# Kernel optimization log

Hardware: AMD Instinct MI355X
Metric: run time of the kernel (lower is better)

Reference implementation:

```python
import jax, jax.numpy as jnp
import numpy as np

WIDTH = 256
FREQS = 10
INPUT_WIDTH = 3 + 3 * 2 * FREQS  # 63


def embed_point(point, freqs):
    # point: [N, 3] -> [N, 3*(1+2*freqs)]
    linear = point[..., None]                                  # [N, 3, 1]
    scales = jnp.exp2(jnp.arange(freqs, dtype=point.dtype))    # [freqs]
    angles = linear * scales                                   # [N, 3, freqs]
    emb = jnp.concatenate((linear, jnp.sin(angles), jnp.cos(angles)), axis=-1)
    return emb.reshape(*point.shape[:-1], 3 * (1 + 2 * freqs))


def _xavier(key, fan_in, fan_out):
    limit = jnp.sqrt(6.0 / (fan_in + fan_out)).astype(jnp.float32)
    return jax.random.uniform(key, (fan_in, fan_out), jnp.float32, -limit, limit)


def setup_inputs() -> dict:
    key = jax.random.key(0)
    keys = jax.random.split(key, 20)
    N = 524288
    point = jax.random.normal(keys[0], (N, 3), dtype=jnp.float32)
    dims = [
        (INPUT_WIDTH, WIDTH), (WIDTH, WIDTH), (WIDTH, WIDTH), (WIDTH, WIDTH),
        (WIDTH, WIDTH), (WIDTH + INPUT_WIDTH, WIDTH), (WIDTH, WIDTH),
        (WIDTH, WIDTH), (WIDTH, 4),
    ]
    inp = {"point": point}
    for i, (fi, fo) in enumerate(dims):
        inp[f"w{i}"] = _xavier(keys[1 + i], fi, fo)
        inp[f"b{i}"] = jnp.zeros((fo,), dtype=jnp.float32)
    return inp


def reference(point, w0, b0, w1, b1, w2, b2, w3, b3, w4, b4,
              w5, b5, w6, b6, w7, b7, w8, b8):
    inp = embed_point(point, FREQS)                 # [N, 63]
    x = jax.nn.relu(inp @ w0 + b0)
    x = jax.nn.relu(x @ w1 + b1)
    x = jax.nn.relu(x @ w2 + b2)
    x = jax.nn.relu(x @ w3 + b3)
    x = jax.nn.relu(x @ w4 + b4)
    x = jax.nn.relu(jnp.concatenate((x, inp), -1) @ w5 + b5)  # skip concat
    x = jax.nn.relu(x @ w6 + b6)
    x = jax.nn.relu(x @ w7 + b7)
    return x @ w8 + b8                              # [N, 4]
```

## Files before the change

kernel.cpp:

```cpp
#include <hip/hip_runtime.h>
#include <math.h>


typedef __attribute__((ext_vector_type(8))) short short8;
typedef __attribute__((ext_vector_type(4))) float f32x4;
typedef __attribute__((ext_vector_type(16))) float f32x16;

struct WPtrs { const float* w[8]; };
struct BPtrs { const float* b[8]; };

#define INV2PI 0.15915494309189533577f

#define PK_L0 0
#define PK_L1 16384
#define PK_L2 81920
#define PK_L3 147456
#define PK_L4 212992
#define PK_L5 278528
#define PK_L6 360448
#define PK_L7 425984
#define PK_W8 491520
#define PK_TOTAL 495616

__device__ __forceinline__ unsigned short f2bf(float v) {
  unsigned u = __float_as_uint(v);
  u = u + 0x7fffu + ((u >> 16) & 1u);
  return (unsigned short)(u >> 16);
}
__device__ __forceinline__ float bf_lo(unsigned u) { return __uint_as_float(u << 16); }
__device__ __forceinline__ float bf_hi(unsigned u) { return __uint_as_float(u & 0xffff0000u); }

__device__ __forceinline__ unsigned cvtpk(float a, float b) {
#if __has_builtin(__builtin_amdgcn_cvt_pk_bf16_f32)
  typedef __attribute__((ext_vector_type(2))) __bf16 bf16x2_t;
  bf16x2_t r = __builtin_amdgcn_cvt_pk_bf16_f32(a, b);
  return __builtin_bit_cast(unsigned, r);
#else
  unsigned ua = __float_as_uint(a);
  ua += 0x7fffu + ((ua >> 16) & 1u);
  unsigned ub = __float_as_uint(b);
  ub += 0x7fffu + ((ub >> 16) & 1u);
#if __has_builtin(__builtin_amdgcn_perm)
  return __builtin_amdgcn_perm(ub, ua, 0x07060302u);
#else
  return (ua >> 16) | (ub & 0xffff0000u);
#endif
#endif
}

__device__ __forceinline__ float fractf_(float x) {
#if __has_builtin(__builtin_amdgcn_fract_f32)
  return __builtin_amdgcn_fract_f32(x);
#else
  return x - floorf(x);
#endif
}
__device__ __forceinline__ float sin_rev(float rev) {
#if __has_builtin(__builtin_amdgcn_sinf)
  return __builtin_amdgcn_sinf(rev);
#else
  return __sinf(rev * 6.283185307179586f);
#endif
}

__device__ __forceinline__ float embval(int f, float c0, float c1, float c2,
                                        float x0, float x1, float x2) {
  if (f >= 63) return 0.0f;
  int d = (f >= 21 ? 1 : 0) + (f >= 42 ? 1 : 0);
  int r = f - d * 21;
  float c = (d == 0) ? c0 : (d == 1 ? c1 : c2);
  float x = (d == 0) ? x0 : (d == 1 ? x1 : x2);
  bool isc = r > 10;
  int e = isc ? (r - 11) : (r - 1);
  float rev = fractf_(ldexpf(x, e) + (isc ? 0.25f : 0.0f));
  float s = sin_rev(rev);
  return (r == 0) ? c : s;
}

__device__ __forceinline__ f32x16 mfma32(short8 a, short8 b, f32x16 c) {
  return __builtin_amdgcn_mfma_f32_32x32x16_bf16(a, b, c, 0, 0, 0);
}
__device__ __forceinline__ f32x4 mfma16(short8 a, short8 b, f32x4 c) {
  return __builtin_amdgcn_mfma_f32_16x16x32_bf16(a, b, c, 0, 0, 0);
}

__global__ void pack_weights(WPtrs W, const float* __restrict__ w8,
                             unsigned short* __restrict__ out) {
  int idx = blockIdx.x * 256 + threadIdx.x;
  if (idx >= PK_TOTAL) return;
  float v;
  if (idx >= PK_W8) {
    int t = idx - PK_W8;
    int j = t >> 8, k = t & 255;
    v = (j < 4) ? w8[k * 4 + j] : 0.0f;
  } else {
    int e = idx & 15;
    int blk = idx >> 4;
    int ch = blk & 255;
    int kkg = blk >> 8;
    int l, kk0;
    if      (kkg < 4)   { l = 0; kk0 = 0;   }
    else if (kkg < 20)  { l = 1; kk0 = 4;   }
    else if (kkg < 36)  { l = 2; kk0 = 20;  }
    else if (kkg < 52)  { l = 3; kk0 = 36;  }
    else if (kkg < 68)  { l = 4; kk0 = 52;  }
    else if (kkg < 88)  { l = 5; kk0 = 68;  }
    else if (kkg < 104) { l = 6; kk0 = 88;  }
    else                { l = 7; kk0 = 104; }
    int k = (kkg - kk0) * 16 + e;
    const int realK[8] = {63, 256, 256, 256, 256, 319, 256, 256};
    v = (k < realK[l]) ? W.w[l][k * 256 + ch] : 0.0f;
  }
  out[idx] = f2bf(v);
}

template <int KKA, int PAB, int KKB, bool RB>
__device__ __forceinline__ void do_layer32(
    const unsigned short* srcA, const unsigned short* srcB,
    const unsigned short* __restrict__ wblk,
    const float* __restrict__ bias,
    unsigned short* dst, int wr, int wc, int n, int h, unsigned swz) {
  f32x16 acc[4][2];
#pragma unroll
  for (int mt = 0; mt < 4; ++mt)
#pragma unroll
    for (int q = 0; q < 4; ++q) {
      f32x4 bq = *reinterpret_cast<const f32x4*>(bias + wr * 128 + mt * 32 + q * 8 + h * 4);
#pragma unroll
      for (int nt = 0; nt < 2; ++nt)
#pragma unroll
        for (int r = 0; r < 4; ++r)
          acc[mt][nt][q * 4 + r] = bq[r];
    }

  const char* wb = (const char*)wblk;
  const unsigned aoff = (unsigned)((wr * 128 + n) * 32 + h * 16);
  const char* rA = (const char*)srcA + (unsigned)((wc * 64 + n) * PAB);

#define LOAD_A(KK, A0, A1, A2, A3) do {                              \
    const char* ap_ = wb + (aoff + (unsigned)((KK) * 8192));         \
    A0 = *reinterpret_cast<const short8*>(ap_);                      \
    A1 = *reinterpret_cast<const short8*>(ap_ + 1024);               \
    A2 = *reinterpret_cast<const short8*>(ap_ + 2048);               \
    A3 = *reinterpret_cast<const short8*>(ap_ + 3072);               \
  } while (0)
#define LOAD_B(KK, B0, B1) do {                                      \
    unsigned off_ = ((unsigned)((KK) * 32 + h * 16)) ^ swz;          \
    const char* p_ = rA + off_;                                      \
    B0 = *reinterpret_cast<const short8*>(p_);                       \
    B1 = *reinterpret_cast<const short8*>(p_ + 32 * PAB);            \
  } while (0)
#define MFMA8(A0, A1, A2, A3, B0, B1) do {                           \
    acc[0][0] = mfma32(A0, B0, acc[0][0]);                           \
    acc[0][1] = mfma32(A0, B1, acc[0][1]);                           \
    acc[1][0] = mfma32(A1, B0, acc[1][0]);                           \
    acc[1][1] = mfma32(A1, B1, acc[1][1]);                           \
    acc[2][0] = mfma32(A2, B0, acc[2][0]);                           \
    acc[2][1] = mfma32(A2, B1, acc[2][1]);                           \
    acc[3][0] = mfma32(A3, B0, acc[3][0]);                           \
    acc[3][1] = mfma32(A3, B1, acc[3][1]);                           \
  } while (0)

  short8 a0e, a1e, a2e, a3e, b0e, b1e;
  short8 a0o, a1o, a2o, a3o, b0o, b1o;
  LOAD_B(0, b0e, b1e);
  LOAD_A(0, a0e, a1e, a2e, a3e);

#pragma unroll
  for (int kk = 0; kk < KKA; ++kk) {
    if ((kk & 1) == 0) {
      if (kk + 1 < KKA) {
        LOAD_B(kk + 1, b0o, b1o);
        LOAD_A(kk + 1, a0o, a1o, a2o, a3o);
      }
      __builtin_amdgcn_sched_barrier(0);
      __builtin_amdgcn_s_setprio(1);
      MFMA8(a0e, a1e, a2e, a3e, b0e, b1e);
      __builtin_amdgcn_s_setprio(0);
      __builtin_amdgcn_sched_barrier(0);
    } else {
      if (kk + 1 < KKA) {
        LOAD_B(kk + 1, b0e, b1e);
        LOAD_A(kk + 1, a0e, a1e, a2e, a3e);
      }
      __builtin_amdgcn_sched_barrier(0);
      __builtin_amdgcn_s_setprio(1);
      MFMA8(a0o, a1o, a2o, a3o, b0o, b1o);
      __builtin_amdgcn_s_setprio(0);
      __builtin_amdgcn_sched_barrier(0);
    }
  }

  if (KKB > 0) {
    const char* rB = (const char*)srcB + (unsigned)((wc * 64 + n) * 128);
#pragma unroll
    for (int kl = 0; kl < KKB; ++kl) {
      const char* ap = wb + (aoff + (unsigned)((KKA + kl) * 8192));
      short8 a0 = *reinterpret_cast<const short8*>(ap);
      short8 a1 = *reinterpret_cast<const short8*>(ap + 1024);
      short8 a2 = *reinterpret_cast<const short8*>(ap + 2048);
      short8 a3 = *reinterpret_cast<const short8*>(ap + 3072);
      unsigned off = ((unsigned)(kl * 32 + h * 16)) ^ swz;
      const char* p = rB + off;
      short8 b0 = *reinterpret_cast<const short8*>(p);
      short8 b1 = *reinterpret_cast<const short8*>(p + 32 * 128);
      __builtin_amdgcn_s_setprio(1);
      MFMA8(a0, a1, a2, a3, b0, b1);
      __builtin_amdgcn_s_setprio(0);
    }
  }
#undef LOAD_A
#undef LOAD_B
#undef MFMA8

  if (RB) __syncthreads();
  char* d0 = (char*)dst + (unsigned)((wc * 64 + n) * 512);
#pragma unroll
  for (int mt = 0; mt < 4; ++mt)
#pragma unroll
    for (int q = 0; q < 4; ++q) {
      unsigned soff = ((unsigned)(wr * 256 + mt * 64 + q * 16 + h * 8)) ^ swz;
      char* sp = d0 + soff;
#pragma unroll
      for (int nt = 0; nt < 2; ++nt) {
        float x0 = fmaxf(acc[mt][nt][q * 4 + 0], 0.0f);
        float x1 = fmaxf(acc[mt][nt][q * 4 + 1], 0.0f);
        float x2 = fmaxf(acc[mt][nt][q * 4 + 2], 0.0f);
        float x3 = fmaxf(acc[mt][nt][q * 4 + 3], 0.0f);
        uint2 pr;
        pr.x = cvtpk(x0, x1);
        pr.y = cvtpk(x2, x3);
        *reinterpret_cast<uint2*>(sp + nt * 16384) = pr;
      }
    }
  __syncthreads();
}

__launch_bounds__(256, 2)
__global__ void mlp_mfma(const float* __restrict__ pts, long N,
                         BPtrs B, const float* __restrict__ b8,
                         const unsigned short* __restrict__ wpk,
                         float* __restrict__ out) {
  extern __shared__ unsigned short smem[];
  unsigned short* act = smem;
  unsigned short* emb = smem + 32768;
  const int tid = threadIdx.x;
  const int w = tid >> 6, lane = tid & 63;
  const int n = lane & 31, h = lane >> 5;
  const int wr = w >> 1, wc = w & 1;
  const unsigned swz = (unsigned)((n & 7) << 4);
  const long pbase = (long)blockIdx.x * 128;

  {
    const int pt = tid >> 1, fg = tid & 1;
    const long pg = pbase + pt;
    float c0 = 0.f, c1 = 0.f, c2 = 0.f;
    if (pg < N) {
      const float* pp = pts + pg * 3;
      c0 = __builtin_nontemporal_load(pp);
      c1 = __builtin_nontemporal_load(pp + 1);
      c2 = __builtin_nontemporal_load(pp + 2);
    }
    float x0 = c0 * INV2PI, x1 = c1 * INV2PI, x2 = c2 * INV2PI;
    const unsigned sw = (unsigned)((pt & 7) << 4);
    char* rowp = (char*)emb + (unsigned)(pt * 128);
#pragma unroll
    for (int jb = 0; jb < 2; ++jb) {
      unsigned pk[8];
#pragma unroll
      for (int i = 0; i < 16; i += 2) {
        int f0 = fg * 32 + jb * 16 + i;
        float v0 = embval(f0,     c0, c1, c2, x0, x1, x2);
        float v1 = embval(f0 + 1, c0, c1, c2, x0, x1, x2);
        pk[i >> 1] = cvtpk(v0, v1);
      }
      unsigned base = (unsigned)(fg * 64 + jb * 32);
      *reinterpret_cast<uint4*>(rowp + (base ^ sw)) =
          uint4{pk[0], pk[1], pk[2], pk[3]};
      *reinterpret_cast<uint4*>(rowp + ((base + 16) ^ sw)) =
          uint4{pk[4], pk[5], pk[6], pk[7]};
    }
  }
  __syncthreads();

  do_layer32<4,  128, 0, false>(emb, nullptr, wpk + PK_L0, B.b[0], act, wr, wc, n, h, swz);
  do_layer32<16, 512, 0, true >(act, nullptr, wpk + PK_L1, B.b[1], act, wr, wc, n, h, swz);
  do_layer32<16, 512, 0, true >(act, nullptr, wpk + PK_L2, B.b[2], act, wr, wc, n, h, swz);
  do_layer32<16, 512, 0, true >(act, nullptr, wpk + PK_L3, B.b[3], act, wr, wc, n, h, swz);
  do_layer32<16, 512, 0, true >(act, nullptr, wpk + PK_L4, B.b[4], act, wr, wc, n, h, swz);
  do_layer32<16, 512, 4, true >(act, emb,     wpk + PK_L5, B.b[5], act, wr, wc, n, h, swz);
  do_layer32<16, 512, 0, true >(act, nullptr, wpk + PK_L6, B.b[6], act, wr, wc, n, h, swz);
  do_layer32<16, 512, 0, true >(act, nullptr, wpk + PK_L7, B.b[7], act, wr, wc, n, h, swz);

  {
    const int l16 = lane & 15, quad = lane >> 4;
    const unsigned short* w8b = wpk + PK_W8 + (unsigned)(l16 * 256 + quad * 8);
    short8 wf[8];
#pragma unroll
    for (int kk = 0; kk < 8; ++kk)
      wf[kk] = *reinterpret_cast<const short8*>(w8b + kk * 32);
    f32x4 bb = *reinterpret_cast<const f32x4*>(b8);
#pragma unroll
    for (int it = 0; it < 2; ++it) {
      const int pt = w * 32 + it * 16 + l16;
      const char* ba = (const char*)act + (unsigned)(pt * 512);
      f32x4 a4 = {0.f, 0.f, 0.f, 0.f};
#pragma unroll
      for (int kk = 0; kk < 8; ++kk) {
        unsigned off = ((unsigned)(kk * 64 + quad * 16)) ^ swz;
        short8 b = *reinterpret_cast<const short8*>(ba + off);
        a4 = mfma16(wf[kk], b, a4);
      }
      if (quad == 0) {
        long pg = pbase + pt;
        f32x4 v = a4 + bb;
        if (pg < N)
          __builtin_nontemporal_store(v, reinterpret_cast<f32x4*>(out + pg * 4));
      }
    }
  }
}

__device__ __forceinline__ unsigned pk2s(float a, float b) {
  return (unsigned)f2bf(a) | ((unsigned)f2bf(b) << 16);
}
__device__ __forceinline__ void fb_seg(const unsigned short* src, int kRows,
                                       const float* __restrict__ wr,
                                       int lane, int ps, float acc[4][16]) {
#pragma unroll 4
  for (int k = 0; k < kRows; ++k) {
    const float* p = wr + k * 256 + lane;
    float w0 = p[0], w1 = p[64], w2 = p[128], w3 = p[192];
    const uint4* xr = reinterpret_cast<const uint4*>(src + ((k << 6) + ps));
    uint4 q0 = xr[0], q1 = xr[1];
    float x[16];
    x[0] = bf_lo(q0.x);  x[1] = bf_hi(q0.x);  x[2] = bf_lo(q0.y);  x[3] = bf_hi(q0.y);
    x[4] = bf_lo(q0.z);  x[5] = bf_hi(q0.z);  x[6] = bf_lo(q0.w);  x[7] = bf_hi(q0.w);
    x[8] = bf_lo(q1.x);  x[9] = bf_hi(q1.x);  x[10] = bf_lo(q1.y); x[11] = bf_hi(q1.y);
    x[12] = bf_lo(q1.z); x[13] = bf_hi(q1.z); x[14] = bf_lo(q1.w); x[15] = bf_hi(q1.w);
#pragma unroll
    for (int pp = 0; pp < 16; ++pp) {
      acc[0][pp] = fmaf(w0, x[pp], acc[0][pp]);
      acc[1][pp] = fmaf(w1, x[pp], acc[1][pp]);
      acc[2][pp] = fmaf(w2, x[pp], acc[2][pp]);
      acc[3][pp] = fmaf(w3, x[pp], acc[3][pp]);
    }
  }
}
__device__ __forceinline__ void fb_layer(const unsigned short* srcA, int kA,
                                         const unsigned short* srcB, int kB,
                                         const float* wrA, const float* wrB,
                                         const float* bias,
                                         unsigned short* dst, int lane, int ps) {
  float acc[4][16];
#pragma unroll
  for (int jt = 0; jt < 4; ++jt) {
    float bb = bias[lane + (jt << 6)];
#pragma unroll
    for (int pp = 0; pp < 16; ++pp) acc[jt][pp] = bb;
  }
  fb_seg(srcA, kA, wrA, lane, ps, acc);
  if (srcB) fb_seg(srcB, kB, wrB, lane, ps, acc);
#pragma unroll
  for (int jt = 0; jt < 4; ++jt) {
    unsigned short* dr = dst + (((lane + (jt << 6)) << 6) + ps);
    float r[16];
#pragma unroll
    for (int pp = 0; pp < 16; ++pp) r[pp] = fmaxf(acc[jt][pp], 0.0f);
    uint4 a, b;
    a.x = pk2s(r[0], r[1]);   a.y = pk2s(r[2], r[3]);
    a.z = pk2s(r[4], r[5]);   a.w = pk2s(r[6], r[7]);
    b.x = pk2s(r[8], r[9]);   b.y = pk2s(r[10], r[11]);
    b.z = pk2s(r[12], r[13]); b.w = pk2s(r[14], r[15]);
    reinterpret_cast<uint4*>(dr)[0] = a;
    reinterpret_cast<uint4*>(dr)[1] = b;
  }
}
__launch_bounds__(256, 2)
__global__ void mlp_fallback(const float* __restrict__ pts, int N,
                             WPtrs W, BPtrs B,
                             const float* __restrict__ w8,
                             const float* __restrict__ b8,
                             float* __restrict__ out) {
  __shared__ unsigned short act[256 * 64];
  __shared__ unsigned short emb[64 * 64];
  const int lane = threadIdx.x & 63;
  const int ps = (threadIdx.x >> 6) << 4;
  const long pbase = (long)blockIdx.x * 64 + ps;
#pragma unroll
  for (int i = 0; i < 16; ++i) {
    int idx = (i << 6) + lane;
    int f = idx >> 4, pp = idx & 15;
    float v = 0.0f;
    if (f < 63) {
      float c = (pbase + pp < N) ? pts[(pbase + pp) * 3 + (f / 21)] : 0.0f;
      float x = c * INV2PI;
      v = embval(f, c, c, c, x, x, x);
    }
    emb[(f << 6) + ps + pp] = f2bf(v);
  }
  fb_layer(emb, 63, nullptr, 0, W.w[0], nullptr, B.b[0], act, lane, ps);
#pragma unroll 1
  for (int l = 1; l <= 4; ++l)
    fb_layer(act, 256, nullptr, 0, W.w[l], nullptr, B.b[l], act, lane, ps);
  fb_layer(act, 256, emb, 63, W.w[5], W.w[5] + 256 * 256, B.b[5], act, lane, ps);
#pragma unroll 1
  for (int l = 6; l <= 7; ++l)
    fb_layer(act, 256, nullptr, 0, W.w[l], nullptr, B.b[l], act, lane, ps);
  {
    const int pp = lane & 15, cc = lane >> 4;
    float a = b8[cc];
#pragma unroll 4
    for (int k = 0; k < 256; ++k)
      a = fmaf(bf_lo((unsigned)act[(k << 6) + ps + pp]), w8[(k << 2) + cc], a);
    if (pbase + pp < N) out[(pbase + pp) * 4 + cc] = a;
  }
}

extern "C" void kernel_launch(void* const* d_in, const int* in_sizes, int n_in,
                              void* d_out, int out_size, void* d_ws, size_t ws_size,
                              hipStream_t stream) {
  const float* pts = (const float*)d_in[0];
  WPtrs W; BPtrs B;
  for (int i = 0; i < 8; ++i) {
    W.w[i] = (const float*)d_in[1 + 2 * i];
    B.b[i] = (const float*)d_in[2 + 2 * i];
  }
  const float* w8 = (const float*)d_in[17];
  const float* b8 = (const float*)d_in[18];
  float* out = (float*)d_out;
  const long N = in_sizes[0] / 3;

  const size_t need = (size_t)PK_TOTAL * sizeof(unsigned short);
  if (ws_size >= need) {
    static hipError_t attr_err = hipFuncSetAttribute(
        reinterpret_cast<const void*>(mlp_mfma),
        hipFuncAttributeMaxDynamicSharedMemorySize, 81920);
    if (attr_err == hipSuccess) {
      unsigned short* wpk = (unsigned short*)d_ws;
      pack_weights<<<1936, 256, 0, stream>>>(W, w8, wpk);
      mlp_mfma<<<(int)((N + 127) / 128), 256, 81920, stream>>>(pts, N, B, b8, wpk, out);
      return;
    }
  }
  mlp_fallback<<<(int)((N + 63) / 64), 256, 0, stream>>>(pts, (int)N, W, B, w8, b8, out);
}
```

Before: 578.6 us.

## Split each layer across eight waves per block with half-height wave tiles

Result: slower. 649.1 us (+12.2%).

```diff
diff --git a/kernel.cpp b/kernel.cpp
--- a/kernel.cpp
+++ b/kernel.cpp
@@ -120,12 +120,12 @@
     const unsigned short* __restrict__ wblk,
     const float* __restrict__ bias,
     unsigned short* dst, int wr, int wc, int n, int h, unsigned swz) {
-  f32x16 acc[4][2];
-#pragma unroll
-  for (int mt = 0; mt < 4; ++mt)
+  f32x16 acc[2][2];
+#pragma unroll
+  for (int mt = 0; mt < 2; ++mt)
 #pragma unroll
     for (int q = 0; q < 4; ++q) {
-      f32x4 bq = *reinterpret_cast<const f32x4*>(bias + wr * 128 + mt * 32 + q * 8 + h * 4);
+      f32x4 bq = *reinterpret_cast<const f32x4*>(bias + wr * 64 + mt * 32 + q * 8 + h * 4);
 #pragma unroll
       for (int nt = 0; nt < 2; ++nt)
 #pragma unroll
@@ -134,15 +134,13 @@
     }
 
   const char* wb = (const char*)wblk;
-  const unsigned aoff = (unsigned)((wr * 128 + n) * 32 + h * 16);
+  const unsigned aoff = (unsigned)(((wr * 64 + n) * 16 + h * 8) * 2);
   const char* rA = (const char*)srcA + (unsigned)((wc * 64 + n) * PAB);
 
-#define LOAD_A(KK, A0, A1, A2, A3) do {                              \
+#define LOAD_A(KK, A0, A1) do {                                      \
     const char* ap_ = wb + (aoff + (unsigned)((KK) * 8192));         \
     A0 = *reinterpret_cast<const short8*>(ap_);                      \
     A1 = *reinterpret_cast<const short8*>(ap_ + 1024);               \
-    A2 = *reinterpret_cast<const short8*>(ap_ + 2048);               \
-    A3 = *reinterpret_cast<const short8*>(ap_ + 3072);               \
   } while (0)
 #define LOAD_B(KK, B0, B1) do {                                      \
     unsigned off_ = ((unsigned)((KK) * 32 + h * 16)) ^ swz;          \
@@ -150,42 +148,38 @@
     B0 = *reinterpret_cast<const short8*>(p_);                       \
     B1 = *reinterpret_cast<const short8*>(p_ + 32 * PAB);            \
   } while (0)
-#define MFMA8(A0, A1, A2, A3, B0, B1) do {                           \
+#define MFMA4(A0, A1, B0, B1) do {                                   \
     acc[0][0] = mfma32(A0, B0, acc[0][0]);                           \
     acc[0][1] = mfma32(A0, B1, acc[0][1]);                           \
     acc[1][0] = mfma32(A1, B0, acc[1][0]);                           \
     acc[1][1] = mfma32(A1, B1, acc[1][1]);                           \
-    acc[2][0] = mfma32(A2, B0, acc[2][0]);                           \
-    acc[2][1] = mfma32(A2, B1, acc[2][1]);                           \
-    acc[3][0] = mfma32(A3, B0, acc[3][0]);                           \
-    acc[3][1] = mfma32(A3, B1, acc[3][1]);                           \
   } while (0)
 
-  short8 a0e, a1e, a2e, a3e, b0e, b1e;
-  short8 a0o, a1o, a2o, a3o, b0o, b1o;
+  short8 a0e, a1e, b0e, b1e;
+  short8 a0o, a1o, b0o, b1o;
   LOAD_B(0, b0e, b1e);
-  LOAD_A(0, a0e, a1e, a2e, a3e);
+  LOAD_A(0, a0e, a1e);
 
 #pragma unroll
   for (int kk = 0; kk < KKA; ++kk) {
     if ((kk & 1) == 0) {
       if (kk + 1 < KKA) {
         LOAD_B(kk + 1, b0o, b1o);
-        LOAD_A(kk + 1, a0o, a1o, a2o, a3o);
+        LOAD_A(kk + 1, a0o, a1o);
       }
       __builtin_amdgcn_sched_barrier(0);
       __builtin_amdgcn_s_setprio(1);
-      MFMA8(a0e, a1e, a2e, a3e, b0e, b1e);
+      MFMA4(a0e, a1e, b0e, b1e);
       __builtin_amdgcn_s_setprio(0);
       __builtin_amdgcn_sched_barrier(0);
     } else {
       if (kk + 1 < KKA) {
         LOAD_B(kk + 1, b0e, b1e);
-        LOAD_A(kk + 1, a0e, a1e, a2e, a3e);
+        LOAD_A(kk + 1, a0e, a1e);
       }
       __builtin_amdgcn_sched_barrier(0);
       __builtin_amdgcn_s_setprio(1);
-      MFMA8(a0o, a1o, a2o, a3o, b0o, b1o);
+      MFMA4(a0o, a1o, b0o, b1o);
       __builtin_amdgcn_s_setprio(0);
       __builtin_amdgcn_sched_barrier(0);
     }
@@ -195,31 +189,29 @@
     const char* rB = (const char*)srcB + (unsigned)((wc * 64 + n) * 128);
 #pragma unroll
     for (int kl = 0; kl < KKB; ++kl) {
-      const char* ap = wb + (aoff + (unsigned)((KKA + kl) * 8192));
-      short8 a0 = *reinterpret_cast<const short8*>(ap);
-      short8 a1 = *reinterpret_cast<const short8*>(ap + 1024);
-      short8 a2 = *reinterpret_cast<const short8*>(ap + 2048);
-      short8 a3 = *reinterpret_cast<const short8*>(ap + 3072);
+      const char* ab2 = wb + (aoff + (unsigned)((KKA + kl) * 8192));
+      short8 a0 = *reinterpret_cast<const short8*>(ab2);
+      short8 a1 = *reinterpret_cast<const short8*>(ab2 + 1024);
       unsigned off = ((unsigned)(kl * 32 + h * 16)) ^ swz;
       const char* p = rB + off;
       short8 b0 = *reinterpret_cast<const short8*>(p);
       short8 b1 = *reinterpret_cast<const short8*>(p + 32 * 128);
       __builtin_amdgcn_s_setprio(1);
-      MFMA8(a0, a1, a2, a3, b0, b1);
+      MFMA4(a0, a1, b0, b1);
       __builtin_amdgcn_s_setprio(0);
     }
   }
 #undef LOAD_A
 #undef LOAD_B
-#undef MFMA8
+#undef MFMA4
 
   if (RB) __syncthreads();
   char* d0 = (char*)dst + (unsigned)((wc * 64 + n) * 512);
 #pragma unroll
-  for (int mt = 0; mt < 4; ++mt)
+  for (int mt = 0; mt < 2; ++mt)
 #pragma unroll
     for (int q = 0; q < 4; ++q) {
-      unsigned soff = ((unsigned)(wr * 256 + mt * 64 + q * 16 + h * 8)) ^ swz;
+      unsigned soff = ((unsigned)(wr * 128 + mt * 64 + q * 16 + h * 8)) ^ swz;
       char* sp = d0 + soff;
 #pragma unroll
       for (int nt = 0; nt < 2; ++nt) {
@@ -236,7 +228,7 @@
   __syncthreads();
 }
 
-__launch_bounds__(256, 2)
+__launch_bounds__(512, 4)
 __global__ void mlp_mfma(const float* __restrict__ pts, long N,
                          BPtrs B, const float* __restrict__ b8,
                          const unsigned short* __restrict__ wpk,
@@ -252,7 +244,7 @@
   const long pbase = (long)blockIdx.x * 128;
 
   {
-    const int pt = tid >> 1, fg = tid & 1;
+    const int pt = tid >> 2, fg = tid & 3;
     const long pg = pbase + pt;
     float c0 = 0.f, c1 = 0.f, c2 = 0.f;
     if (pg < N) {
@@ -262,24 +254,20 @@
       c2 = __builtin_nontemporal_load(pp + 2);
     }
     float x0 = c0 * INV2PI, x1 = c1 * INV2PI, x2 = c2 * INV2PI;
+    unsigned pk[8];
+#pragma unroll
+    for (int i = 0; i < 16; i += 2) {
+      int f0 = fg * 16 + i;
+      float v0 = embval(f0,     c0, c1, c2, x0, x1, x2);
+      float v1 = embval(f0 + 1, c0, c1, c2, x0, x1, x2);
+      pk[i >> 1] = cvtpk(v0, v1);
+    }
     const unsigned sw = (unsigned)((pt & 7) << 4);
     char* rowp = (char*)emb + (unsigned)(pt * 128);
-#pragma unroll
-    for (int jb = 0; jb < 2; ++jb) {
-      unsigned pk[8];
-#pragma unroll
-      for (int i = 0; i < 16; i += 2) {
-        int f0 = fg * 32 + jb * 16 + i;
-        float v0 = embval(f0,     c0, c1, c2, x0, x1, x2);
-        float v1 = embval(f0 + 1, c0, c1, c2, x0, x1, x2);
-        pk[i >> 1] = cvtpk(v0, v1);
-      }
-      unsigned base = (unsigned)(fg * 64 + jb * 32);
-      *reinterpret_cast<uint4*>(rowp + (base ^ sw)) =
-          uint4{pk[0], pk[1], pk[2], pk[3]};
-      *reinterpret_cast<uint4*>(rowp + ((base + 16) ^ sw)) =
-          uint4{pk[4], pk[5], pk[6], pk[7]};
-    }
+    *reinterpret_cast<uint4*>(rowp + (((unsigned)(fg * 32)) ^ sw)) =
+        uint4{pk[0], pk[1], pk[2], pk[3]};
+    *reinterpret_cast<uint4*>(rowp + (((unsigned)(fg * 32 + 16)) ^ sw)) =
+        uint4{pk[4], pk[5], pk[6], pk[7]};
   }
   __syncthreads();
 
@@ -300,23 +288,20 @@
     for (int kk = 0; kk < 8; ++kk)
       wf[kk] = *reinterpret_cast<const short8*>(w8b + kk * 32);
     f32x4 bb = *reinterpret_cast<const f32x4*>(b8);
-#pragma unroll
-    for (int it = 0; it < 2; ++it) {
-      const int pt = w * 32 + it * 16 + l16;
-      const char* ba = (const char*)act + (unsigned)(pt * 512);
-      f32x4 a4 = {0.f, 0.f, 0.f, 0.f};
-#pragma unroll
-      for (int kk = 0; kk < 8; ++kk) {
-        unsigned off = ((unsigned)(kk * 64 + quad * 16)) ^ swz;
-        short8 b = *reinterpret_cast<const short8*>(ba + off);
-        a4 = mfma16(wf[kk], b, a4);
-      }
-      if (quad == 0) {
-        long pg = pbase + pt;
-        f32x4 v = a4 + bb;
-        if (pg < N)
-          __builtin_nontemporal_store(v, reinterpret_cast<f32x4*>(out + pg * 4));
-      }
+    const int pt = w * 16 + l16;
+    const char* ba = (const char*)act + (unsigned)(pt * 512);
+    f32x4 a4 = {0.f, 0.f, 0.f, 0.f};
+#pragma unroll
+    for (int kk = 0; kk < 8; ++kk) {
+      unsigned off = ((unsigned)(kk * 64 + quad * 16)) ^ swz;
+      short8 b = *reinterpret_cast<const short8*>(ba + off);
+      a4 = mfma16(wf[kk], b, a4);
+    }
+    if (quad == 0) {
+      long pg = pbase + pt;
+      f32x4 v = a4 + bb;
+      if (pg < N)
+        __builtin_nontemporal_store(v, reinterpret_cast<f32x4*>(out + pg * 4));
     }
   }
 }
@@ -439,7 +424,7 @@
     if (attr_err == hipSuccess) {
       unsigned short* wpk = (unsigned short*)d_ws;
       pack_weights<<<1936, 256, 0, stream>>>(W, w8, wpk);
-      mlp_mfma<<<(int)((N + 127) / 128), 256, 81920, stream>>>(pts, N, B, b8, wpk, out);
+      mlp_mfma<<<(int)((N + 127) / 128), 512, 81920, stream>>>(pts, N, B, b8, wpk, out);
       return;
     }
   }
```
